# Kernel tuning notes

Hardware: AMD Instinct MI355X
Metric: run time of the kernel (lower is better)

Reference implementation:

```python
import jax, jax.numpy as jnp
import numpy as np

TH, TW = 64, 64        # template_size (image shape)
OH, OW = 256, 256      # out_size
K = 3                  # spline order
PAD = 4                # hardcoded padding in module
OFF = PAD - (K + 1) // 2          # = 2
CX_OFF = (OH - TH) // 2           # centering_offset[0] = 96
CY_OFF = (OW - TW) // 2           # centering_offset[1] = 96
BATCH = 1024


def bspline3(p):
    # fast cubic B-spline basis, p: (B,) -> (B, 4)
    return jnp.stack([
        p ** 3 / 6,
        -p ** 3 / 2 + p ** 2 / 2 + p / 2 + 1.0 / 6,
        p ** 3 / 2 - p ** 2 + 2.0 / 3,
        (1 - p) ** 3 / 6,
    ], axis=-1)


def setup_inputs() -> dict:
    key = jax.random.key(0)
    k1, k2, k3 = jax.random.split(key, 3)
    coeffs = jax.random.normal(k1, (TH + 2 * PAD, TW + 2 * PAD), jnp.float32)
    x = (jax.random.normal(k2, (BATCH, 1, 1, 1), jnp.float32) - 0.5) * 10
    y = (jax.random.normal(k3, (BATCH, 1, 1, 1), jnp.float32) - 0.5) * 10
    return {"coeffs": coeffs, "x": x, "y": y}


def reference(coeffs, x, y):
    B = x.shape[0]
    # integer pixel shift (floor) and subpixel remainder
    px = jnp.floor(x[:, 0, 0, 0]).astype(jnp.int32)  # (B,)
    py = jnp.floor(y[:, 0, 0, 0]).astype(jnp.int32)  # (B,)
    sx = jnp.remainder(x[:, 0, 0, 0], 1.0)           # (B,)
    sy = jnp.remainder(y[:, 0, 0, 0], 1.0)           # (B,)

    bx = bspline3(sx)  # (B,4) basis along rows (i index)
    by = bspline3(sy)  # (B,4) basis along cols (j index)

    # (4,4,TH+1,TW+1) shifted coefficient windows
    slices = jnp.stack([
        jnp.stack([coeffs[i + OFF:i + OFF + TH + 1, j + OFF:j + OFF + TW + 1]
                   for j in range(K + 1)])
        for i in range(K + 1)])
    # blended template: (B, TH+1, TW+1)
    template = jnp.einsum('bi,bj,ijrc->brc', bx, by, slices)

    bi = jnp.arange(B)[:, None, None]

    # scatter along columns (dim 3 in torch): x_a[b, r, idx_a] = template[b, r, c]
    col = jnp.arange(TW + 1)
    idx_a = jnp.clip(col[None, None, :] + py[:, None, None] + CY_OFF + 1, 0, OW + 1)  # (B,1,TW+1)
    ri = jnp.arange(TH + 1)[None, :, None]
    x_a = jnp.zeros((B, OH + 2, OW + 2), template.dtype)
    x_a = x_a.at[bi, ri, idx_a].set(template)

    # scatter along rows (dim 2 in torch): x_b[b, idx_b, c] = x_a[b, r, c]
    row = jnp.arange(OH + 2)
    idx_b = jnp.clip(row[None, :, None] + px[:, None, None] + CX_OFF + 1, 0, OH + 1)  # (B,OH+2,1)
    ci = jnp.arange(OW + 2)[None, None, :]
    x_b = jnp.zeros_like(x_a).at[bi, idx_b, ci].set(x_a)

    return x_b[:, 1:-1, 1:-1][:, None]  # (B,1,OH,OW)
```

## Files before the change

kernel.cpp:

```cpp
#include <hip/hip_runtime.h>


#define CW 72

typedef float f4 __attribute__((ext_vector_type(4)));

__device__ __forceinline__ void st_nt(float* p, f4 v) {
    __builtin_nontemporal_store(v, reinterpret_cast<f4*>(p));
}

__global__ __launch_bounds__(256) void spline2d_fused3(
    const float* __restrict__ coeffs,
    const float* __restrict__ x,
    const float* __restrict__ y,
    float* __restrict__ out)
{
    __shared__ float rb[16][80];

    const int blk    = blockIdx.x;
    const int b      = blk >> 4;
    const int seg    = blk & 15;
    const int Rstart = seg << 4;

    const float xv = x[b];
    const float fx = floorf(xv);
    const int   R0 = (int)fx + 96;

    const int t         = threadIdx.x;
    const int rowInPass = t >> 6;
    const int col4      = (t & 63) << 2;

    float* __restrict__ obase =
        out + ((size_t)b << 16) + ((size_t)Rstart << 8);
    const f4 z4 = {0.f, 0.f, 0.f, 0.f};

    if (R0 > Rstart + 15 || R0 + 64 < Rstart) {
#pragma unroll
        for (int u = 0; u < 4; ++u)
            st_nt(obase + (u << 10) + (rowInPass << 8) + col4, z4);
        return;
    }

    const float yv = y[b];
    const float fy = floorf(yv);
    const int   C0 = (int)fy + 96;
    const float sx = xv - fx, sy = yv - fy;

    float wx0, wx1, wx2, wx3, wy0, wy1, wy2, wy3;
    {
        const float p = sx, p2 = p * p, p3 = p2 * p, q = 1.0f - p;
        wx0 = p3 * (1.0f / 6.0f);
        wx1 = -0.5f * p3 + 0.5f * p2 + 0.5f * p + (1.0f / 6.0f);
        wx2 = 0.5f * p3 - p2 + (2.0f / 3.0f);
        wx3 = q * q * q * (1.0f / 6.0f);
    }
    {
        const float p = sy, p2 = p * p, p3 = p2 * p, q = 1.0f - p;
        wy0 = p3 * (1.0f / 6.0f);
        wy1 = -0.5f * p3 + 0.5f * p2 + 0.5f * p + (1.0f / 6.0f);
        wy2 = 0.5f * p3 - p2 + (2.0f / 3.0f);
        wy3 = q * q * q * (1.0f / 6.0f);
    }

    {
        const int slot   = t >> 4;
        const int lane16 = t & 15;
        const int r      = Rstart + slot - R0;
        const bool rok   = (unsigned)r <= 64u;
        const float* p0base = coeffs + (r + 2) * CW + 2;
#pragma unroll
        for (int it = 0; it < 5; ++it) {
            const int k = lane16 + (it << 4);
            if (k < 68) {
                float v = 0.0f;
                if (rok) {
                    const float* p0 = p0base + k;
                    v = p0[0] * wx0 + p0[CW] * wx1 + p0[2 * CW] * wx2 + p0[3 * CW] * wx3;
                }
                rb[slot][k] = v;
            }
        }
    }
    __syncthreads();

    const int c0 = col4 - C0;
#pragma unroll
    for (int u = 0; u < 4; ++u) {
        const int slot = (u << 2) + rowInPass;
        const int r    = Rstart + slot - R0;
        f4 v = z4;
        if ((unsigned)r <= 64u && c0 >= -3 && c0 <= 64) {
#pragma unroll
            for (int m = 0; m < 4; ++m) {
                const int c = c0 + m;
                if ((unsigned)c <= 64u) {
                    v[m] = rb[slot][c] * wy0 + rb[slot][c + 1] * wy1 +
                           rb[slot][c + 2] * wy2 + rb[slot][c + 3] * wy3;
                }
            }
        }
        st_nt(obase + (u << 10) + (rowInPass << 8) + col4, v);
    }
}

extern "C" void kernel_launch(void* const* d_in, const int* in_sizes, int n_in,
                              void* d_out, int out_size, void* d_ws, size_t ws_size,
                              hipStream_t stream) {
    const float* coeffs = (const float*)d_in[0];
    const float* x      = (const float*)d_in[1];
    const float* y      = (const float*)d_in[2];
    float* out = (float*)d_out;

    const int batch = in_sizes[1];
    spline2d_fused3<<<batch * 16, 256, 0, stream>>>(coeffs, x, y, out);
}
```

Measured before the change: 268.9 us.

## Use one block per batch image with full row-blended template in LDS

Moves from 16 blocks per image (each covering 16 output rows) to one block per image. The block computes the whole 65x68 row-blended template into shared memory once, then loops over all 256 output rows, writing zeros or the column-blended values. This removes the launch and per-block overhead and the recomputation of weights across 16 blocks. In exchange, each block computes all template rows even when few are visible, uses about 17 KB of LDS, and launches far fewer blocks, which lowers parallelism for a store-bound kernel.

```diff
diff --git a/kernel.cpp b/kernel.cpp
--- a/kernel.cpp
+++ b/kernel.cpp
@@ -9,40 +9,20 @@
     __builtin_nontemporal_store(v, reinterpret_cast<f4*>(p));
 }
 
-__global__ __launch_bounds__(256) void spline2d_fused3(
+__global__ __launch_bounds__(256) void spline2d_fused4(
     const float* __restrict__ coeffs,
     const float* __restrict__ x,
     const float* __restrict__ y,
     float* __restrict__ out)
 {
-    __shared__ float rb[16][80];
+    __shared__ float rb[65][68];
 
-    const int blk    = blockIdx.x;
-    const int b      = blk >> 4;
-    const int seg    = blk & 15;
-    const int Rstart = seg << 4;
+    const int b = blockIdx.x;
 
     const float xv = x[b];
-    const float fx = floorf(xv);
+    const float yv = y[b];
+    const float fx = floorf(xv), fy = floorf(yv);
     const int   R0 = (int)fx + 96;
-
-    const int t         = threadIdx.x;
-    const int rowInPass = t >> 6;
-    const int col4      = (t & 63) << 2;
-
-    float* __restrict__ obase =
-        out + ((size_t)b << 16) + ((size_t)Rstart << 8);
-    const f4 z4 = {0.f, 0.f, 0.f, 0.f};
-
-    if (R0 > Rstart + 15 || R0 + 64 < Rstart) {
-#pragma unroll
-        for (int u = 0; u < 4; ++u)
-            st_nt(obase + (u << 10) + (rowInPass << 8) + col4, z4);
-        return;
-    }
-
-    const float yv = y[b];
-    const float fy = floorf(yv);
     const int   C0 = (int)fy + 96;
     const float sx = xv - fx, sy = yv - fy;
 
@@ -62,44 +42,48 @@
         wy3 = q * q * q * (1.0f / 6.0f);
     }
 
-    {
-        const int slot   = t >> 4;
-        const int lane16 = t & 15;
-        const int r      = Rstart + slot - R0;
-        const bool rok   = (unsigned)r <= 64u;
-        const float* p0base = coeffs + (r + 2) * CW + 2;
+    const int t    = threadIdx.x;
+    const int w    = t >> 6;
+    const int lane = t & 63;
+
 #pragma unroll
-        for (int it = 0; it < 5; ++it) {
-            const int k = lane16 + (it << 4);
-            if (k < 68) {
-                float v = 0.0f;
-                if (rok) {
-                    const float* p0 = p0base + k;
-                    v = p0[0] * wx0 + p0[CW] * wx1 + p0[2 * CW] * wx2 + p0[3 * CW] * wx3;
-                }
-                rb[slot][k] = v;
+    for (int pass = 0; pass < 17; ++pass) {
+        const int r = (pass << 2) + w;
+        if (r <= 64) {
+            const float* p0 = coeffs + (r + 2) * CW + 2;
+            rb[r][lane] = p0[lane] * wx0 + p0[lane + CW] * wx1 +
+                          p0[lane + 2 * CW] * wx2 + p0[lane + 3 * CW] * wx3;
+            if (lane < 4) {
+                const int k = 64 + lane;
+                rb[r][k] = p0[k] * wx0 + p0[k + CW] * wx1 +
+                           p0[k + 2 * CW] * wx2 + p0[k + 3 * CW] * wx3;
             }
         }
     }
     __syncthreads();
 
-    const int c0 = col4 - C0;
-#pragma unroll
-    for (int u = 0; u < 4; ++u) {
-        const int slot = (u << 2) + rowInPass;
-        const int r    = Rstart + slot - R0;
+    float* __restrict__ obase = out + ((size_t)b << 16);
+    const int  col4 = lane << 2;
+    const int  c0   = col4 - C0;
+    const bool cin  = (c0 >= -3 && c0 <= 64);
+    const f4   z4   = {0.f, 0.f, 0.f, 0.f};
+
+#pragma unroll 8
+    for (int it = 0; it < 64; ++it) {
+        const int row = (it << 2) + w;
+        const int r   = row - R0;
         f4 v = z4;
-        if ((unsigned)r <= 64u && c0 >= -3 && c0 <= 64) {
+        if ((unsigned)r <= 64u && cin) {
 #pragma unroll
             for (int m = 0; m < 4; ++m) {
                 const int c = c0 + m;
                 if ((unsigned)c <= 64u) {
-                    v[m] = rb[slot][c] * wy0 + rb[slot][c + 1] * wy1 +
-                           rb[slot][c + 2] * wy2 + rb[slot][c + 3] * wy3;
+                    v[m] = rb[r][c] * wy0 + rb[r][c + 1] * wy1 +
+                           rb[r][c + 2] * wy2 + rb[r][c + 3] * wy3;
                 }
             }
         }
-        st_nt(obase + (u << 10) + (rowInPass << 8) + col4, v);
+        st_nt(obase + (row << 8) + col4, v);
     }
 }
 
@@ -112,5 +96,5 @@
     float* out = (float*)d_out;
 
     const int batch = in_sizes[1];
-    spline2d_fused3<<<batch * 16, 256, 0, stream>>>(coeffs, x, y, out);
+    spline2d_fused4<<<batch, 256, 0, stream>>>(coeffs, x, y, out);
 }
```

Result: slower. 277.9 us (+3.4%).
